# Performance work log

Measured on AMD Instinct MI355X. Metric: run time of the kernel, lower is better.

The kernel has to match this reference:

```python
import jax, jax.numpy as jnp
import numpy as np

V, R, A, C, T = 50000, 5, 8, 32, 32  # vertices, radial, angular, in-channels, templates
DELTA = 2                             # rotation_delta -> n_rotations = A // DELTA = 4


def setup_inputs() -> dict:
    key = jax.random.key(0)
    ks = jax.random.split(key, 6)
    signal = jax.random.normal(ks[0], (V, C), jnp.float32)
    bc_idx = jax.random.randint(ks[1], (V, R, A, 3), 0, V, dtype=jnp.int32)
    w = jax.random.uniform(ks[2], (V, R, A, 3), jnp.float32)
    bc_w = w / jnp.sum(w, axis=-1, keepdims=True)  # barycentric weights sum to 1
    templ1 = jax.random.normal(ks[3], (T, R, A, C), jnp.float32) * 0.05
    bias1 = jnp.zeros((T,), jnp.float32)
    templ2 = jax.random.normal(ks[4], (T, R, A, T), jnp.float32) * 0.05
    bias2 = jnp.zeros((T,), jnp.float32)
    return {"signal": signal, "bc_idx": bc_idx, "bc_w": bc_w,
            "templ1": templ1, "bias1": bias1, "templ2": templ2, "bias2": bias2}


def _conv_dirac(x, bc_idx, bc_w, templ, bias):
    """Dirac intrinsic surface convolution.
    x: [V, Cin]; bc_idx/bc_w: [V, R, A, 3]; templ: [T, R, A, Cin] -> [V, n_rot, T]."""
    # Barycentric interpolation of the mesh signal at template vertices.
    gathered = x[bc_idx]                                   # [V, R, A, 3, Cin]
    interp = jnp.einsum('vrai,vraic->vrac', bc_w, gathered)  # [V, R, A, Cin]
    n_rot = A // DELTA
    # Rotating the patch by +s angular steps == correlating with templ rolled by +s.
    rot_t = jnp.stack([jnp.roll(templ, r * DELTA, axis=2) for r in range(n_rot)])  # [n_rot, T, R, A, Cin]
    return jnp.einsum('vrac,ntrac->vnt', interp, rot_t) + bias  # [V, n_rot, T]


def _amp(x):
    # AngularMaxPooling: max over the rotation axis.
    return jnp.max(x, axis=1)


def reference(signal, bc_idx, bc_w, templ1, bias1, templ2, bias2):
    s = jax.nn.relu(_conv_dirac(signal, bc_idx, bc_w, templ1, bias1))  # conv1 (relu)
    s = _amp(s)                                                        # [V, T]
    s = _conv_dirac(s, bc_idx, bc_w, templ2, bias2)                    # conv2 (linear)
    s = _amp(s)                                                        # [V, T]
    # input_dim == amt_templates -> no rescale branch; residual add + output relu
    return jax.nn.relu(s + signal)
```

## Files before the change

### kernel.cpp

```cpp
#include <hip/hip_runtime.h>
#include <hip/hip_bf16.h>

#define VN 50000
#define RN 5
#define AN 8
#define CN 32
#define NB 8
#define MT 32

typedef short bf16x8  __attribute__((ext_vector_type(8)));
typedef short bf16x16 __attribute__((ext_vector_type(16)));
typedef float f32x4   __attribute__((ext_vector_type(4)));

__device__ __forceinline__ float b2f(short s) {
    union { unsigned u; float f; } cv;
    cv.u = ((unsigned)(unsigned short)s) << 16;
    return cv.f;
}
__device__ __forceinline__ short f2b(float f) {
    union { float f; unsigned u; } cv; cv.f = f;
    unsigned r = cv.u + 0x7fff + ((cv.u >> 16) & 1);
    return (short)(r >> 16);
}

__global__ void pack_x(const float* __restrict__ x, __hip_bfloat16* __restrict__ xb, int n4) {
    int i = blockIdx.x * blockDim.x + threadIdx.x;
    if (i >= n4) return;
    float4 v = ((const float4*)x)[i];
    ushort4 o;
    o.x = (unsigned short)f2b(v.x);
    o.y = (unsigned short)f2b(v.y);
    o.z = (unsigned short)f2b(v.z);
    o.w = (unsigned short)f2b(v.w);
    ((ushort4*)xb)[i] = o;
}

__global__ void build_Bp(const float* __restrict__ t1, const float* __restrict__ t2,
                         __hip_bfloat16* __restrict__ B1, __hip_bfloat16* __restrict__ B2) {
    int m = blockIdx.x * blockDim.x + threadIdx.x;
    if (m >= RN * AN * NB * 64 * 8) return;
    int j = m & 7;
    int lane = (m >> 3) & 63;
    int nb = (m >> 9) & 7;
    int kstep = m >> 12;
    int c = ((lane >> 4) << 3) + j;
    int r = kstep >> 3, a = kstep & 7;
    int nt = nb * 16 + (lane & 15);
    int n = nt >> 5, t = nt & 31;
    int asrc = (a - 2 * n + 8) & 7;
    int src = ((t * RN + r) * AN + asrc) * CN + c;
    ((unsigned short*)B1)[m] = (unsigned short)f2b(t1[src]);
    ((unsigned short*)B2)[m] = (unsigned short)f2b(t2[src]);
}

template<bool FIRST>
__global__ __launch_bounds__(128)
void conv_fused(const __hip_bfloat16* __restrict__ xb,
                const int*   __restrict__ bc_idx,
                const float* __restrict__ bc_w,
                const __hip_bfloat16* __restrict__ Bp,
                const float* __restrict__ bias,
                const float* __restrict__ signal,
                __hip_bfloat16* __restrict__ out_bf,
                float* __restrict__ out_f)
{
    __shared__ __align__(16) unsigned char smraw[16384];
    const int tid = threadIdx.x;
    const int wid = tid >> 6;
    const int lane = tid & 63;
    const int vbase = blockIdx.x * MT;
    const unsigned short* xs = (const unsigned short*)xb;

    const int arow = lane & 15;
    const int c0q = lane >> 4;

    f32x4 acc[2][4];
#pragma unroll
    for (int mi = 0; mi < 2; ++mi)
#pragma unroll
        for (int j = 0; j < 4; ++j) acc[mi][j] = (f32x4)(0.f);

    for (int r = 0; r < RN; ++r) {
        if (r) __syncthreads();

#pragma unroll
        for (int k = 0; k < 4; ++k) {
            int id = tid + k * 128;
            int vl = id >> 4, a = (id >> 1) & 7, h = id & 1;
            int vg = vbase + vl;
            int vc = vg < VN ? vg : VN - 1;
            const int*   ip = bc_idx + (size_t)vc * 120 + r * 24 + a * 3;
            const float* wp = bc_w   + (size_t)vc * 120 + r * 24 + a * 3;
            int   i0 = __builtin_nontemporal_load(ip);
            int   i1 = __builtin_nontemporal_load(ip + 1);
            int   i2 = __builtin_nontemporal_load(ip + 2);
            float w0 = __builtin_nontemporal_load(wp);
            float w1 = __builtin_nontemporal_load(wp + 1);
            float w2 = __builtin_nontemporal_load(wp + 2);
            bf16x16 g0 = *(const bf16x16*)(xs + (size_t)i0 * CN + h * 16);
            bf16x16 g1 = *(const bf16x16*)(xs + (size_t)i1 * CN + h * 16);
            bf16x16 g2 = *(const bf16x16*)(xs + (size_t)i2 * CN + h * 16);
            bf16x8 ch[2];
#pragma unroll
            for (int j = 0; j < 16; ++j) {
                float f = fmaf(w0, b2f(g0[j]), fmaf(w1, b2f(g1[j]), w2 * b2f(g2[j])));
                ch[j >> 3][j & 7] = f2b(f);
            }
#pragma unroll
            for (int qq = 0; qq < 2; ++qq) {
                int q = h * 2 + qq;
                int baddr = vl * 512 + ((a * 64 + q * 16) ^ ((vl & 7) << 4));
                *(bf16x8*)(smraw + baddr) = ch[qq];
            }
        }
        __syncthreads();

#pragma unroll
        for (int ks = 0; ks < 8; ++ks) {
            bf16x8 af[2];
#pragma unroll
            for (int mi = 0; mi < 2; ++mi) {
                int row = mi * 16 + arow;
                int baddr = row * 512 + ((ks * 64 + c0q * 16) ^ ((row & 7) << 4));
                af[mi] = *(const bf16x8*)(smraw + baddr);
            }
            int gks = r * 8 + ks;
#pragma unroll
            for (int j = 0; j < 4; ++j) {
                int nb = wid * 4 + j;
                bf16x8 bfr = *(const bf16x8*)((const unsigned short*)Bp +
                                ((size_t)(gks * NB + nb) * 64 + lane) * 8);
                acc[0][j] = __builtin_amdgcn_mfma_f32_16x16x32_bf16(af[0], bfr, acc[0][j], 0, 0, 0);
                acc[1][j] = __builtin_amdgcn_mfma_f32_16x16x32_bf16(af[1], bfr, acc[1][j], 0, 0, 0);
            }
        }
    }

    __syncthreads();
    f32x4* redp = (f32x4*)smraw;
#pragma unroll
    for (int mi = 0; mi < 2; ++mi)
#pragma unroll
        for (int q = 0; q < 2; ++q) {
            f32x4 pm;
#pragma unroll
            for (int rg = 0; rg < 4; ++rg)
                pm[rg] = fmaxf(acc[mi][q][rg], acc[mi][q + 2][rg]);
            redp[((wid * 2 + mi) * 2 + q) * 64 + lane] = pm;
        }
    __syncthreads();

    const int colD = lane & 15;
    const int rbase = (lane >> 4) << 2;
#pragma unroll
    for (int q = 0; q < 2; ++q) {
        f32x4 m0 = redp[((0 * 2 + wid) * 2 + q) * 64 + lane];
        f32x4 m1 = redp[((1 * 2 + wid) * 2 + q) * 64 + lane];
        int t = q * 16 + colD;
        float b = bias[t];
#pragma unroll
        for (int rg = 0; rg < 4; ++rg) {
            int vv = vbase + wid * 16 + rbase + rg;
            if (vv < VN) {
                float val = fmaxf(m0[rg], m1[rg]) + b;
                if (FIRST) {
                    ((unsigned short*)out_bf)[vv * CN + t] =
                        (unsigned short)f2b(fmaxf(val, 0.f));
                } else {
                    val += __builtin_nontemporal_load(signal + vv * CN + t);
                    __builtin_nontemporal_store(fmaxf(val, 0.f), out_f + vv * CN + t);
                }
            }
        }
    }
}

extern "C" void kernel_launch(void* const* d_in, const int* in_sizes, int n_in,
                              void* d_out, int out_size, void* d_ws, size_t ws_size,
                              hipStream_t stream) {
    const float* signal = (const float*)d_in[0];
    const int*   bc_idx = (const int*)d_in[1];
    const float* bc_w   = (const float*)d_in[2];
    const float* t1     = (const float*)d_in[3];
    const float* b1     = (const float*)d_in[4];
    const float* t2     = (const float*)d_in[5];
    const float* b2     = (const float*)d_in[6];
    float* out = (float*)d_out;

    __hip_bfloat16* ws = (__hip_bfloat16*)d_ws;
    __hip_bfloat16* xb  = ws;
    __hip_bfloat16* s1  = ws + VN * CN;
    __hip_bfloat16* Bp1 = ws + 2 * VN * CN;
    __hip_bfloat16* Bp2 = Bp1 + RN * AN * NB * 64 * 8;

    pack_x<<<(VN * CN / 4 + 255) / 256, 256, 0, stream>>>(signal, xb, VN * CN / 4);
    build_Bp<<<(RN * AN * NB * 64 * 8) / 256, 256, 0, stream>>>(t1, t2, Bp1, Bp2);

    int blocks = (VN + MT - 1) / MT;
    conv_fused<true ><<<blocks, 128, 0, stream>>>(xb, bc_idx, bc_w, Bp1, b1, nullptr, s1, nullptr);
    conv_fused<false><<<blocks, 128, 0, stream>>>(s1, bc_idx, bc_w, Bp2, b2, signal, nullptr, out);
}
```

Before: 261.0 us.

## Software-pipeline neighbor gathers across radial rings with vectorized index loads

Changes the thread-to-work mapping so each thread handles one vertex, one half of the channels and four angles. Index and weight rows are fetched as 16-byte vectors and prefetched one to two rings ahead in double-buffered registers. The gathers for ring r+1 are issued before the MFMA loop for ring r, so the random gather latency overlaps with matrix compute. This raises register pressure (12 bf16x16 gather buffers plus the prefetch arrays), which the launch bounds of 2 may push into spills. It also adds a barrier at the end of every ring.

```diff
diff --git a/kernel.cpp b/kernel.cpp
--- a/kernel.cpp
+++ b/kernel.cpp
@@ -11,6 +11,7 @@
 typedef short bf16x8  __attribute__((ext_vector_type(8)));
 typedef short bf16x16 __attribute__((ext_vector_type(16)));
 typedef float f32x4   __attribute__((ext_vector_type(4)));
+typedef int   i32x4   __attribute__((ext_vector_type(4)));
 
 __device__ __forceinline__ float b2f(short s) {
     union { unsigned u; float f; } cv;
@@ -54,7 +55,7 @@
 }
 
 template<bool FIRST>
-__global__ __launch_bounds__(128)
+__global__ __launch_bounds__(128, 2)
 void conv_fused(const __hip_bfloat16* __restrict__ xb,
                 const int*   __restrict__ bc_idx,
                 const float* __restrict__ bc_w,
@@ -68,9 +69,15 @@
     const int tid = threadIdx.x;
     const int wid = tid >> 6;
     const int lane = tid & 63;
+    const int vl = tid & 31;
+    const int h  = (tid >> 5) & 1;
     const int vbase = blockIdx.x * MT;
     const unsigned short* xs = (const unsigned short*)xb;
 
+    int vg = vbase + vl;
+    int vc = vg < VN ? vg : VN - 1;
+    const size_t ibase = (size_t)vc * 120 + wid * 12;
+
     const int arow = lane & 15;
     const int c0q = lane >> 4;
 
@@ -80,40 +87,70 @@
 #pragma unroll
         for (int j = 0; j < 4; ++j) acc[mi][j] = (f32x4)(0.f);
 
+    i32x4 I[2][3];
+    f32x4 Wv[2][3];
+    bf16x16 G[12];
+
+#pragma unroll
+    for (int q = 0; q < 3; ++q) {
+        I[0][q]  = __builtin_nontemporal_load((const i32x4*)(bc_idx + ibase) + q);
+        I[1][q]  = __builtin_nontemporal_load((const i32x4*)(bc_idx + ibase + 24) + q);
+        Wv[0][q] = __builtin_nontemporal_load((const f32x4*)(bc_w  + ibase) + q);
+    }
+    __builtin_amdgcn_sched_barrier(0);
+#pragma unroll
+    for (int e = 0; e < 12; ++e) {
+        int idx = I[0][e >> 2][e & 3];
+        G[e] = *(const bf16x16*)(xs + (size_t)idx * CN + h * 16);
+    }
+    __builtin_amdgcn_sched_barrier(0);
+
+#pragma unroll
     for (int r = 0; r < RN; ++r) {
-        if (r) __syncthreads();
-
-#pragma unroll
-        for (int k = 0; k < 4; ++k) {
-            int id = tid + k * 128;
-            int vl = id >> 4, a = (id >> 1) & 7, h = id & 1;
-            int vg = vbase + vl;
-            int vc = vg < VN ? vg : VN - 1;
-            const int*   ip = bc_idx + (size_t)vc * 120 + r * 24 + a * 3;
-            const float* wp = bc_w   + (size_t)vc * 120 + r * 24 + a * 3;
-            int   i0 = __builtin_nontemporal_load(ip);
-            int   i1 = __builtin_nontemporal_load(ip + 1);
-            int   i2 = __builtin_nontemporal_load(ip + 2);
-            float w0 = __builtin_nontemporal_load(wp);
-            float w1 = __builtin_nontemporal_load(wp + 1);
-            float w2 = __builtin_nontemporal_load(wp + 2);
-            bf16x16 g0 = *(const bf16x16*)(xs + (size_t)i0 * CN + h * 16);
-            bf16x16 g1 = *(const bf16x16*)(xs + (size_t)i1 * CN + h * 16);
-            bf16x16 g2 = *(const bf16x16*)(xs + (size_t)i2 * CN + h * 16);
+        if (r + 2 < RN) {
+#pragma unroll
+            for (int q = 0; q < 3; ++q)
+                I[r & 1][q] = __builtin_nontemporal_load(
+                    (const i32x4*)(bc_idx + ibase + (r + 2) * 24) + q);
+        }
+        if (r + 1 < RN) {
+#pragma unroll
+            for (int q = 0; q < 3; ++q)
+                Wv[(r + 1) & 1][q] = __builtin_nontemporal_load(
+                    (const f32x4*)(bc_w + ibase + (r + 1) * 24) + q);
+        }
+        __builtin_amdgcn_sched_barrier(0);
+
+#pragma unroll
+        for (int aa = 0; aa < 4; ++aa) {
+            const int a = wid * 4 + aa;
+            float w0 = Wv[r & 1][(aa * 3 + 0) >> 2][(aa * 3 + 0) & 3];
+            float w1 = Wv[r & 1][(aa * 3 + 1) >> 2][(aa * 3 + 1) & 3];
+            float w2 = Wv[r & 1][(aa * 3 + 2) >> 2][(aa * 3 + 2) & 3];
             bf16x8 ch[2];
 #pragma unroll
             for (int j = 0; j < 16; ++j) {
-                float f = fmaf(w0, b2f(g0[j]), fmaf(w1, b2f(g1[j]), w2 * b2f(g2[j])));
+                float f = fmaf(w0, b2f(G[aa * 3 + 0][j]),
+                         fmaf(w1, b2f(G[aa * 3 + 1][j]),
+                               w2 * b2f(G[aa * 3 + 2][j])));
                 ch[j >> 3][j & 7] = f2b(f);
             }
 #pragma unroll
             for (int qq = 0; qq < 2; ++qq) {
-                int q = h * 2 + qq;
-                int baddr = vl * 512 + ((a * 64 + q * 16) ^ ((vl & 7) << 4));
+                int baddr = vl * 512 + ((a * 64 + h * 32 + qq * 16) ^ ((vl & 7) << 4));
                 *(bf16x8*)(smraw + baddr) = ch[qq];
             }
         }
         __syncthreads();
+
+        if (r + 1 < RN) {
+#pragma unroll
+            for (int e = 0; e < 12; ++e) {
+                int idx = I[(r + 1) & 1][e >> 2][e & 3];
+                G[e] = *(const bf16x16*)(xs + (size_t)idx * CN + h * 16);
+            }
+            __builtin_amdgcn_sched_barrier(0);
+        }
 
 #pragma unroll
         for (int ks = 0; ks < 8; ++ks) {
@@ -134,9 +171,9 @@
                 acc[1][j] = __builtin_amdgcn_mfma_f32_16x16x32_bf16(af[1], bfr, acc[1][j], 0, 0, 0);
             }
         }
-    }
-
-    __syncthreads();
+        __syncthreads();
+    }
+
     f32x4* redp = (f32x4*)smraw;
 #pragma unroll
     for (int mi = 0; mi < 2; ++mi)
```

Result: faster. 228.2 us (-12.6%).
